# Performance work log

Hardware: AMD Instinct MI355X
Metric: run time of the kernel (lower is better)

## Reference

```python
import jax, jax.numpy as jnp
import numpy as np

N = 100000   # n_nodes
E = 1600000  # n_edges (avg degree 16)
F = 128      # in_feats
H = 3        # num_heads
D = 16       # out_feats per head
NEG_SLOPE = 0.2


def setup_inputs() -> dict:
    key = jax.random.key(0)
    k = jax.random.split(key, 6)
    x = jax.random.normal(k[0], (N, F), jnp.float32)
    # fc weight [H*D, F] (torch Linear convention), xavier-normal-ish scale
    W = jax.random.normal(k[1], (H * D, F), jnp.float32) * np.float32((2.0 / (F + H * D)) ** 0.5)
    attn_l = jax.random.normal(k[2], (1, H, D), jnp.float32) * 0.1
    attn_r = jax.random.normal(k[3], (1, H, D), jnp.float32) * 0.1
    linear_comb = jnp.full((N,), 0.5, jnp.float32)
    src = jax.random.randint(k[4], (E,), 0, N, dtype=jnp.int32)
    dst = jax.random.randint(k[5], (E,), 0, N, dtype=jnp.int32)
    return dict(x=x, W=W, attn_l=attn_l, attn_r=attn_r, linear_comb=linear_comb, src=src, dst=dst)


def reference(x, W, attn_l, attn_r, linear_comb, src, dst):
    # fc + reshape to [N, H, D]
    feat = (x @ W.T).reshape(N, H, D)
    # per-node attention logits [N, H]
    el = jnp.einsum('nhd,ohd->nh', feat, attn_l)
    er = jnp.einsum('nhd,ohd->nh', feat, attn_r)
    # edge scores: u_add_v + leaky relu  [E, H]
    e = el[src] + er[dst]
    e = jnp.where(e > 0, e, NEG_SLOPE * e)
    # edge_softmax: segment softmax over incoming edges (grouped by dst)
    emax = jax.ops.segment_max(e, dst, num_segments=N)
    emax = jnp.where(jnp.isfinite(emax), emax, 0.0)  # empty segments -> 0
    ex = jnp.exp(e - emax[dst])
    denom = jax.ops.segment_sum(ex, dst, num_segments=N)
    a = ex / denom[dst]
    # u_mul_e + mailbox sum: scatter-sum of attention-weighted src features
    msg = jax.ops.segment_sum(feat[src] * a[..., None], dst, num_segments=N)  # [N, H, D]
    # linear-combination residual gate per node
    lin = linear_comb[:, None, None]
    return (1.0 - lin) * msg + lin * feat
```

## Files before the change

kernel.cpp:

```cpp
#include <hip/hip_runtime.h>

constexpr int F = 128;
constexpr int H = 3;
constexpr int D = 16;
constexpr int C = H * D;
constexpr int RS = 32;
constexpr int BKT = 256;
constexpr int CHUNK = 2048;
constexpr int MAXNB = 512;
#define NEG_SLOPE 0.2f

__device__ __forceinline__ unsigned short f2bf(float f) {
    unsigned u = __float_as_uint(f);
    u += 0x7fffu + ((u >> 16) & 1u);
    return (unsigned short)(u >> 16);
}
__device__ __forceinline__ float bflo(unsigned u) { return __uint_as_float(u << 16); }
__device__ __forceinline__ float bfhi(unsigned u) { return __uint_as_float(u & 0xffff0000u); }

__global__ __launch_bounds__(256) void feat_kernel(
    const float* __restrict__ x, const float* __restrict__ W,
    const float* __restrict__ attn_l, const float* __restrict__ attn_r,
    float* __restrict__ packed, float* __restrict__ er, int N)
{
    __shared__ float Ws[C][F + 4];
    const int tid = threadIdx.x;

    for (int i = tid; i < C * F / 4; i += 256) {
        int c = i >> 5, k4 = i & 31;
        float4 v = *reinterpret_cast<const float4*>(&W[c * F + k4 * 4]);
        *reinterpret_cast<float4*>(&Ws[c][k4 * 4]) = v;
    }
    __syncthreads();

    const int nl = tid >> 2;
    const int cg = tid & 3;
    const int n = blockIdx.x * 64 + nl;
    const int c0 = cg * 12;
    if (n >= N) return;

    const float* xrow = &x[(size_t)n * F];
    float acc[12];
#pragma unroll
    for (int j = 0; j < 12; ++j) acc[j] = 0.f;

    for (int k4 = 0; k4 < F / 4; ++k4) {
        float4 xv = *reinterpret_cast<const float4*>(&xrow[k4 * 4]);
#pragma unroll
        for (int j = 0; j < 12; ++j) {
            float4 wv = *reinterpret_cast<const float4*>(&Ws[c0 + j][k4 * 4]);
            acc[j] += xv.x * wv.x + xv.y * wv.y + xv.z * wv.z + xv.w * wv.w;
        }
    }
    unsigned up[6];
#pragma unroll
    for (int i = 0; i < 6; ++i)
        up[i] = (unsigned)f2bf(acc[2 * i]) | ((unsigned)f2bf(acc[2 * i + 1]) << 16);
    uint2* prow = reinterpret_cast<uint2*>(packed + (size_t)n * RS + cg * 6);
    prow[0] = make_uint2(up[0], up[1]);
    prow[1] = make_uint2(up[2], up[3]);
    prow[2] = make_uint2(up[4], up[5]);

    float pl[H] = {0.f, 0.f, 0.f}, pr[H] = {0.f, 0.f, 0.f};
#pragma unroll
    for (int j = 0; j < 12; ++j) {
        int c = c0 + j;
        int h = c >> 4;
        pl[h] += acc[j] * attn_l[c];
        pr[h] += acc[j] * attn_r[c];
    }
#pragma unroll
    for (int h = 0; h < H; ++h) {
        pl[h] += __shfl_xor(pl[h], 1);
        pl[h] += __shfl_xor(pl[h], 2);
        pr[h] += __shfl_xor(pr[h], 1);
        pr[h] += __shfl_xor(pr[h], 2);
    }
    if (cg == 0) {
        *reinterpret_cast<float4*>(packed + (size_t)n * RS + 24) =
            make_float4(pl[0], pl[1], pl[2], 0.f);
        er[(size_t)n * H + 0] = pr[0];
        er[(size_t)n * H + 1] = pr[1];
        er[(size_t)n * H + 2] = pr[2];
    }
}

__global__ __launch_bounds__(256) void p1_count_kernel(
    const int* __restrict__ dst, int* __restrict__ counts, int E, int EB, int NB)
{
    __shared__ int hist[MAXNB];
    const int tid = threadIdx.x;
    for (int b = tid; b < NB; b += 256) hist[b] = 0;
    __syncthreads();
    const int base = blockIdx.x * CHUNK;
#pragma unroll
    for (int k = 0; k < CHUNK / 256; ++k) {
        int e = base + k * 256 + tid;
        if (e < E) atomicAdd(&hist[dst[e] >> 8], 1);
    }
    __syncthreads();
    for (int b = tid; b < NB; b += 256)
        counts[(size_t)b * EB + blockIdx.x] = hist[b];
}

__global__ __launch_bounds__(256) void scanA_kernel(
    const int* __restrict__ a, int* __restrict__ partials, int T)
{
    __shared__ int red[256];
    const int tid = threadIdx.x;
    const int base = blockIdx.x * 1024;
    int s = 0;
#pragma unroll
    for (int k = 0; k < 4; ++k) {
        int i = base + k * 256 + tid;
        if (i < T) s += a[i];
    }
    red[tid] = s;
    __syncthreads();
#pragma unroll
    for (int d = 128; d > 0; d >>= 1) {
        if (tid < d) red[tid] += red[tid + d];
        __syncthreads();
    }
    if (tid == 0) partials[blockIdx.x] = red[0];
}

__global__ __launch_bounds__(512) void scanB_kernel(int* __restrict__ partials, int B)
{
    __shared__ int s[512];
    const int tid = threadIdx.x;
    int v = (tid < B) ? partials[tid] : 0;
    s[tid] = v;
    __syncthreads();
    for (int d = 1; d < 512; d <<= 1) {
        int t = (tid >= d) ? s[tid - d] : 0;
        __syncthreads();
        s[tid] += t;
        __syncthreads();
    }
    if (tid < B) partials[tid] = s[tid] - v;
}

__global__ __launch_bounds__(256) void scanC_kernel(
    int* __restrict__ a, const int* __restrict__ partials, int T)
{
    __shared__ int s[256];
    const int tid = threadIdx.x;
    const int idx0 = blockIdx.x * 1024 + tid * 4;
    int e0 = 0, e1 = 0, e2 = 0, e3 = 0;
    if (idx0     < T) e0 = a[idx0];
    if (idx0 + 1 < T) e1 = a[idx0 + 1];
    if (idx0 + 2 < T) e2 = a[idx0 + 2];
    if (idx0 + 3 < T) e3 = a[idx0 + 3];
    int ls = e0 + e1 + e2 + e3;
    s[tid] = ls;
    __syncthreads();
    for (int d = 1; d < 256; d <<= 1) {
        int t = (tid >= d) ? s[tid - d] : 0;
        __syncthreads();
        s[tid] += t;
        __syncthreads();
    }
    int ex = s[tid] - ls + partials[blockIdx.x];
    if (idx0     < T) a[idx0]     = ex;
    if (idx0 + 1 < T) a[idx0 + 1] = ex + e0;
    if (idx0 + 2 < T) a[idx0 + 2] = ex + e0 + e1;
    if (idx0 + 3 < T) a[idx0 + 3] = ex + e0 + e1 + e2;
}

__global__ __launch_bounds__(256) void p3_scatter_kernel(
    const int* __restrict__ src, const int* __restrict__ dst,
    const int* __restrict__ counts, uint2* __restrict__ pairs,
    int E, int EB, int NB)
{
    __shared__ int cur[MAXNB];
    const int tid = threadIdx.x;
    for (int b = tid; b < NB; b += 256)
        cur[b] = counts[(size_t)b * EB + blockIdx.x];
    __syncthreads();
    const int base = blockIdx.x * CHUNK;
#pragma unroll
    for (int k = 0; k < CHUNK / 256; ++k) {
        int e = base + k * 256 + tid;
        if (e < E) {
            int d = dst[e];
            int p = atomicAdd(&cur[d >> 8], 1);
            pairs[p] = make_uint2((unsigned)src[e], (unsigned)d);
        }
    }
}

__global__ __launch_bounds__(256) void p4_refine_kernel(
    const uint2* __restrict__ pairs, const int* __restrict__ counts,
    int* __restrict__ off, int* __restrict__ srcs,
    int N, int E, int EB, int NB)
{
    __shared__ int cnt[BKT];
    __shared__ int s[BKT];
    __shared__ int pref[BKT];
    const int tid = threadIdx.x;
    const int b = blockIdx.x;
    const int start = counts[(size_t)b * EB];
    const int end = (b == NB - 1) ? E : counts[(size_t)(b + 1) * EB];

    cnt[tid] = 0;
    __syncthreads();
    for (int e = start + tid; e < end; e += 256)
        atomicAdd(&cnt[pairs[e].y & (BKT - 1)], 1);
    __syncthreads();

    int v = cnt[tid];
    s[tid] = v;
    __syncthreads();
    for (int d = 1; d < 256; d <<= 1) {
        int t = (tid >= d) ? s[tid - d] : 0;
        __syncthreads();
        s[tid] += t;
        __syncthreads();
    }
    int ex = s[tid] - v;
    pref[tid] = ex;
    int dg = b * BKT + tid;
    if (dg <= N) off[dg] = start + ex;
    __syncthreads();

    for (int e = start + tid; e < end; e += 256) {
        uint2 pr = pairs[e];
        int d = pr.y & (BKT - 1);
        int slot = start + atomicAdd(&pref[d], 1);
        srcs[slot] = (int)pr.x;
    }
}

__global__ __launch_bounds__(256) void gather_kernel(
    const int* __restrict__ off, const int* __restrict__ srcs,
    const float* __restrict__ packed, const float* __restrict__ er,
    const float* __restrict__ lin, float* __restrict__ out, int N)
{
    const int tid = threadIdx.x;
    const int nl = tid >> 2;
    const int cg = tid & 3;
    const int n = blockIdx.x * 64 + nl;
    if (n >= N) return;
    const int cbase = cg * 12;
    const int hA = cbase >> 4;
    const int hB = (cbase + 11) >> 4;
    const int jb0 = 16 - (cbase & 15);
    const int jb = jb0 > 12 ? 12 : jb0;
    const bool twoHeads = (hB != hA);

    const float ernA = er[(size_t)n * H + hA];
    const float ernB = er[(size_t)n * H + hB];

    float acc[12];
#pragma unroll
    for (int j = 0; j < 12; ++j) acc[j] = 0.f;
    float denA = 0.f, denB = 0.f;

    const int start = off[n];
    const int end = off[n + 1];
    int e = start;

#define EDGE_BODY(SRC)                                                         \
    {                                                                          \
        const float* row = packed + (size_t)(SRC) * RS;                        \
        float4 ev = *reinterpret_cast<const float4*>(row + 24);                \
        float elA = hA == 0 ? ev.x : (hA == 1 ? ev.y : ev.z);                  \
        float tA = elA + ernA;                                                 \
        tA = tA > 0.f ? tA : NEG_SLOPE * tA;                                   \
        float wA = __expf(tA);                                                 \
        denA += wA;                                                            \
        float wB = wA;                                                         \
        if (twoHeads) {                                                        \
            float elB = hB == 1 ? ev.y : ev.z;                                 \
            float tB = elB + ernB;                                             \
            tB = tB > 0.f ? tB : NEG_SLOPE * tB;                               \
            wB = __expf(tB);                                                   \
            denB += wB;                                                        \
        }                                                                      \
        const uint2* fp = reinterpret_cast<const uint2*>(row + cg * 6);        \
        uint2 q0 = fp[0], q1 = fp[1], q2 = fp[2];                              \
        unsigned uu[6] = {q0.x, q0.y, q1.x, q1.y, q2.x, q2.y};                 \
        _Pragma("unroll")                                                      \
        for (int i = 0; i < 6; ++i) {                                          \
            float wlo = (2 * i < jb) ? wA : wB;                                \
            float whi = (2 * i + 1 < jb) ? wA : wB;                            \
            acc[2 * i]     += wlo * bflo(uu[i]);                               \
            acc[2 * i + 1] += whi * bfhi(uu[i]);                               \
        }                                                                      \
    }

    for (; e + 2 <= end; e += 2) {
        int s0 = srcs[e];
        int s1 = srcs[e + 1];
        EDGE_BODY(s0);
        EDGE_BODY(s1);
    }
    if (e < end) {
        int s0 = srcs[e];
        EDGE_BODY(s0);
    }
#undef EDGE_BODY

    const float l = lin[n];
    const float om = 1.f - l;
    float invA = denA > 0.f ? 1.f / denA : 0.f;
    float invB = twoHeads ? (denB > 0.f ? 1.f / denB : 0.f) : invA;

    const float* myrow = packed + (size_t)n * RS;
    const uint2* mp = reinterpret_cast<const uint2*>(myrow + cg * 6);
    uint2 m0 = mp[0], m1 = mp[1], m2 = mp[2];
    unsigned mu[6] = {m0.x, m0.y, m1.x, m1.y, m2.x, m2.y};

    float o[12];
#pragma unroll
    for (int i = 0; i < 6; ++i) {
        float ilo = (2 * i < jb) ? invA : invB;
        float ihi = (2 * i + 1 < jb) ? invA : invB;
        o[2 * i]     = om * (acc[2 * i] * ilo) + l * bflo(mu[i]);
        o[2 * i + 1] = om * (acc[2 * i + 1] * ihi) + l * bfhi(mu[i]);
    }
#pragma unroll
    for (int j = 0; j < 12; j += 4) {
        *reinterpret_cast<float4*>(&out[(size_t)n * C + cbase + j]) =
            make_float4(o[j], o[j + 1], o[j + 2], o[j + 3]);
    }
}

extern "C" void kernel_launch(void* const* d_in, const int* in_sizes, int n_in,
                              void* d_out, int out_size, void* d_ws, size_t ws_size,
                              hipStream_t stream)
{
    const float* x      = (const float*)d_in[0];
    const float* W      = (const float*)d_in[1];
    const float* attn_l = (const float*)d_in[2];
    const float* attn_r = (const float*)d_in[3];
    const float* lin    = (const float*)d_in[4];
    const int*   src    = (const int*)d_in[5];
    const int*   dst    = (const int*)d_in[6];
    const int N = in_sizes[4];
    const int E = in_sizes[5];
    float* out = (float*)d_out;

    const int NB = (N + BKT - 1) / BKT;
    const int EB = (E + CHUNK - 1) / CHUNK;
    const int T  = NB * EB;
    const int SBlk = (T + 1023) / 1024;

    float* packed   = (float*)d_ws;
    float* er       = packed + (size_t)N * RS;
    uint2* pairs    = (uint2*)(er + (size_t)N * H);
    int*   counts   = (int*)(pairs + E);
    int*   partials = counts + T;
    int*   off      = partials + 1024;
    int*   srcs     = off + (N + 1);

    feat_kernel<<<(N + 63) / 64, 256, 0, stream>>>(
        x, W, attn_l, attn_r, packed, er, N);
    p1_count_kernel<<<EB, 256, 0, stream>>>(dst, counts, E, EB, NB);
    scanA_kernel<<<SBlk, 256, 0, stream>>>(counts, partials, T);
    scanB_kernel<<<1, 512, 0, stream>>>(partials, SBlk);
    scanC_kernel<<<SBlk, 256, 0, stream>>>(counts, partials, T);
    p3_scatter_kernel<<<EB, 256, 0, stream>>>(src, dst, counts, pairs, E, EB, NB);
    p4_refine_kernel<<<NB, 256, 0, stream>>>(pairs, counts, off, srcs, N, E, EB, NB);
    gather_kernel<<<(N + 63) / 64, 256, 0, stream>>>(
        off, srcs, packed, er, lin, out, N);
}
```

Baseline: 231.7 us.

## Pack edge pairs into 32-bit words, unroll gather by four, enlarge chunk

The intermediate (src, dst) pairs become a single 32-bit word holding a 17-bit source index and the 8-bit local destination, which halves the scatter and refine traffic. The gather loop is unrolled to four edges with every row load issued before any compute, so more memory requests are in flight. CHUNK is doubled to 4096, giving fewer edge blocks and a smaller counts/scan array. The packing assumes N fits in 17 bits (up to 131072), and the unrolled loop raises register pressure.

```diff
diff --git a/kernel.cpp b/kernel.cpp
--- a/kernel.cpp
+++ b/kernel.cpp
@@ -6,7 +6,7 @@
 constexpr int C = H * D;
 constexpr int RS = 32;
 constexpr int BKT = 256;
-constexpr int CHUNK = 2048;
+constexpr int CHUNK = 4096;
 constexpr int MAXNB = 512;
 #define NEG_SLOPE 0.2f
 
@@ -170,7 +170,7 @@
 
 __global__ __launch_bounds__(256) void p3_scatter_kernel(
     const int* __restrict__ src, const int* __restrict__ dst,
-    const int* __restrict__ counts, uint2* __restrict__ pairs,
+    const int* __restrict__ counts, unsigned* __restrict__ pairs,
     int E, int EB, int NB)
 {
     __shared__ int cur[MAXNB];
@@ -185,13 +185,13 @@
         if (e < E) {
             int d = dst[e];
             int p = atomicAdd(&cur[d >> 8], 1);
-            pairs[p] = make_uint2((unsigned)src[e], (unsigned)d);
+            pairs[p] = (unsigned)src[e] | ((unsigned)(d & (BKT - 1)) << 17);
         }
     }
 }
 
 __global__ __launch_bounds__(256) void p4_refine_kernel(
-    const uint2* __restrict__ pairs, const int* __restrict__ counts,
+    const unsigned* __restrict__ pairs, const int* __restrict__ counts,
     int* __restrict__ off, int* __restrict__ srcs,
     int N, int E, int EB, int NB)
 {
@@ -206,7 +206,7 @@
     cnt[tid] = 0;
     __syncthreads();
     for (int e = start + tid; e < end; e += 256)
-        atomicAdd(&cnt[pairs[e].y & (BKT - 1)], 1);
+        atomicAdd(&cnt[pairs[e] >> 17], 1);
     __syncthreads();
 
     int v = cnt[tid];
@@ -225,10 +225,9 @@
     __syncthreads();
 
     for (int e = start + tid; e < end; e += 256) {
-        uint2 pr = pairs[e];
-        int d = pr.y & (BKT - 1);
-        int slot = start + atomicAdd(&pref[d], 1);
-        srcs[slot] = (int)pr.x;
+        unsigned pr = pairs[e];
+        int slot = start + atomicAdd(&pref[pr >> 17], 1);
+        srcs[slot] = (int)(pr & 0x1FFFFu);
     }
 }
 
@@ -261,26 +260,22 @@
     const int end = off[n + 1];
     int e = start;
 
-#define EDGE_BODY(SRC)                                                         \
+#define COMPUTE(EV, U0, U1, U2, U3, U4, U5)                                    \
     {                                                                          \
-        const float* row = packed + (size_t)(SRC) * RS;                        \
-        float4 ev = *reinterpret_cast<const float4*>(row + 24);                \
-        float elA = hA == 0 ? ev.x : (hA == 1 ? ev.y : ev.z);                  \
+        float elA = hA == 0 ? (EV).x : (hA == 1 ? (EV).y : (EV).z);            \
         float tA = elA + ernA;                                                 \
         tA = tA > 0.f ? tA : NEG_SLOPE * tA;                                   \
         float wA = __expf(tA);                                                 \
         denA += wA;                                                            \
         float wB = wA;                                                         \
         if (twoHeads) {                                                        \
-            float elB = hB == 1 ? ev.y : ev.z;                                 \
+            float elB = hB == 1 ? (EV).y : (EV).z;                             \
             float tB = elB + ernB;                                             \
             tB = tB > 0.f ? tB : NEG_SLOPE * tB;                               \
             wB = __expf(tB);                                                   \
             denB += wB;                                                        \
         }                                                                      \
-        const uint2* fp = reinterpret_cast<const uint2*>(row + cg * 6);        \
-        uint2 q0 = fp[0], q1 = fp[1], q2 = fp[2];                              \
-        unsigned uu[6] = {q0.x, q0.y, q1.x, q1.y, q2.x, q2.y};                 \
+        unsigned uu[6] = {U0, U1, U2, U3, U4, U5};                             \
         _Pragma("unroll")                                                      \
         for (int i = 0; i < 6; ++i) {                                          \
             float wlo = (2 * i < jb) ? wA : wB;                                \
@@ -290,17 +285,38 @@
         }                                                                      \
     }
 
-    for (; e + 2 <= end; e += 2) {
+    for (; e + 4 <= end; e += 4) {
+        int s0 = srcs[e], s1 = srcs[e + 1], s2 = srcs[e + 2], s3 = srcs[e + 3];
+        const float* r0 = packed + (size_t)s0 * RS;
+        const float* r1 = packed + (size_t)s1 * RS;
+        const float* r2 = packed + (size_t)s2 * RS;
+        const float* r3 = packed + (size_t)s3 * RS;
+        float4 ev0 = *reinterpret_cast<const float4*>(r0 + 24);
+        float4 ev1 = *reinterpret_cast<const float4*>(r1 + 24);
+        float4 ev2 = *reinterpret_cast<const float4*>(r2 + 24);
+        float4 ev3 = *reinterpret_cast<const float4*>(r3 + 24);
+        const uint2* f0 = reinterpret_cast<const uint2*>(r0 + cg * 6);
+        const uint2* f1 = reinterpret_cast<const uint2*>(r1 + cg * 6);
+        const uint2* f2 = reinterpret_cast<const uint2*>(r2 + cg * 6);
+        const uint2* f3 = reinterpret_cast<const uint2*>(r3 + cg * 6);
+        uint2 a0 = f0[0], b0 = f0[1], c0 = f0[2];
+        uint2 a1 = f1[0], b1 = f1[1], c1 = f1[2];
+        uint2 a2 = f2[0], b2 = f2[1], c2 = f2[2];
+        uint2 a3 = f3[0], b3 = f3[1], c3 = f3[2];
+        COMPUTE(ev0, a0.x, a0.y, b0.x, b0.y, c0.x, c0.y);
+        COMPUTE(ev1, a1.x, a1.y, b1.x, b1.y, c1.x, c1.y);
+        COMPUTE(ev2, a2.x, a2.y, b2.x, b2.y, c2.x, c2.y);
+        COMPUTE(ev3, a3.x, a3.y, b3.x, b3.y, c3.x, c3.y);
+    }
+    for (; e < end; ++e) {
         int s0 = srcs[e];
-        int s1 = srcs[e + 1];
-        EDGE_BODY(s0);
-        EDGE_BODY(s1);
-    }
-    if (e < end) {
-        int s0 = srcs[e];
-        EDGE_BODY(s0);
-    }
-#undef EDGE_BODY
+        const float* r0 = packed + (size_t)s0 * RS;
+        float4 ev0 = *reinterpret_cast<const float4*>(r0 + 24);
+        const uint2* f0 = reinterpret_cast<const uint2*>(r0 + cg * 6);
+        uint2 a0 = f0[0], b0 = f0[1], c0 = f0[2];
+        COMPUTE(ev0, a0.x, a0.y, b0.x, b0.y, c0.x, c0.y);
+    }
+#undef COMPUTE
 
     const float l = lin[n];
     const float om = 1.f - l;
@@ -347,13 +363,13 @@
     const int T  = NB * EB;
     const int SBlk = (T + 1023) / 1024;
 
-    float* packed   = (float*)d_ws;
-    float* er       = packed + (size_t)N * RS;
-    uint2* pairs    = (uint2*)(er + (size_t)N * H);
-    int*   counts   = (int*)(pairs + E);
-    int*   partials = counts + T;
-    int*   off      = partials + 1024;
-    int*   srcs     = off + (N + 1);
+    float*    packed   = (float*)d_ws;
+    float*    er       = packed + (size_t)N * RS;
+    unsigned* pairs    = (unsigned*)(er + (size_t)N * H);
+    int*      counts   = (int*)(pairs + E);
+    int*      partials = counts + T;
+    int*      off      = partials + 1024;
+    int*      srcs     = off + (N + 1);
 
     feat_kernel<<<(N + 63) / 64, 256, 0, stream>>>(
         x, W, attn_l, attn_r, packed, er, N);
```

Result: faster. 227.1 us (-2.0%).
